# Performance work log

Hardware: AMD Instinct MI355X
Metric: run time of the kernel (lower is better)

## Reference

```python
import jax, jax.numpy as jnp
import numpy as np

D_MODEL = 1024
NHEAD = 16
D_K = D_MODEL // NHEAD


def setup_inputs() -> dict:
    key = jax.random.key(0)
    ks = jax.random.split(key, 11)
    B, S = 4, 2048
    s = 1.0 / np.sqrt(D_MODEL)
    return {
        "query": jax.random.normal(ks[0], (B, S, D_MODEL), jnp.float32),
        "key": jax.random.normal(ks[1], (B, S, D_MODEL), jnp.float32),
        "value": jax.random.normal(ks[2], (B, S, D_MODEL), jnp.float32),
        "wq": jax.random.normal(ks[3], (D_MODEL, D_MODEL), jnp.float32) * s,
        "bq": jnp.zeros((D_MODEL,), jnp.float32),
        "wk": jax.random.normal(ks[4], (D_MODEL, D_MODEL), jnp.float32) * s,
        "bk": jnp.zeros((D_MODEL,), jnp.float32),
        "wv": jax.random.normal(ks[5], (D_MODEL, D_MODEL), jnp.float32) * s,
        "bv": jnp.zeros((D_MODEL,), jnp.float32),
        "wo": jax.random.normal(ks[6], (D_MODEL, D_MODEL), jnp.float32) * s,
        "bo": jnp.zeros((D_MODEL,), jnp.float32),
    }


def reference(query, key, value, wq, bq, wk, bk, wv, bv, wo, bo):
    B, Sq, _ = query.shape
    Sk = key.shape[1]
    scale = 1.0 / np.sqrt(D_K).astype(np.float32)
    # projections, split into heads: [B, H, S, d_k]
    Q = (query @ wq.T + bq).reshape(B, Sq, NHEAD, D_K).transpose(0, 2, 1, 3)
    K = (key @ wk.T + bk).reshape(B, Sk, NHEAD, D_K).transpose(0, 2, 1, 3)
    V = (value @ wv.T + bv).reshape(B, Sk, NHEAD, D_K).transpose(0, 2, 1, 3)
    scores = jnp.einsum('bhqd,bhkd->bhqk', Q, K) * scale
    attn = jax.nn.softmax(scores, axis=-1)  # dropout p=0 (eval)
    ctx = jnp.einsum('bhqk,bhkd->bhqd', attn, V)
    ctx = ctx.transpose(0, 2, 1, 3).reshape(B, Sq, D_MODEL)
    return ctx @ wo.T + bo
```

## Files before the change

### kernel.cpp

```cpp
#include <hip/hip_runtime.h>
#include <math.h>

#define D_MODEL 1024
#define NHEAD   16
#define DK      64
#define BATCH   4
#define SEQ     2048
#define MROWS   8192

typedef __attribute__((ext_vector_type(4)))  float f32x4;
typedef __attribute__((ext_vector_type(16))) float f32x16;
typedef __attribute__((ext_vector_type(8)))  short bf16x8;

#define QSCALE 0.18033688011112042f

__device__ __forceinline__ unsigned int cvt_pk_bf16(float lo, float hi) {
  unsigned int r;
  asm("v_cvt_pk_bf16_f32 %0, %1, %2" : "=v"(r) : "v"(lo), "v"(hi));
  return r;
}

__global__ __launch_bounds__(256) void cvt_all(
    const float* __restrict__ q, const float* __restrict__ k, const float* __restrict__ v,
    const float* __restrict__ wq, const float* __restrict__ wk,
    const float* __restrict__ wv, const float* __restrict__ wo,
    unsigned short* __restrict__ qb, unsigned short* __restrict__ kb,
    unsigned short* __restrict__ vb, unsigned short* __restrict__ wqb,
    unsigned short* __restrict__ wkb, unsigned short* __restrict__ wvb,
    unsigned short* __restrict__ wob) {
  const int bid = blockIdx.x;
  const float* src; unsigned short* dst; int off;
  if      (bid < 4096)  { src = q;  dst = qb;  off = bid; }
  else if (bid < 8192)  { src = k;  dst = kb;  off = bid - 4096; }
  else if (bid < 12288) { src = v;  dst = vb;  off = bid - 8192; }
  else if (bid < 12800) { src = wq; dst = wqb; off = bid - 12288; }
  else if (bid < 13312) { src = wk; dst = wkb; off = bid - 12800; }
  else if (bid < 13824) { src = wv; dst = wvb; off = bid - 13312; }
  else                  { src = wo; dst = wob; off = bid - 13824; }
  const size_t i = (size_t)off * 256 + threadIdx.x;
  const float4* p = (const float4*)src + i * 2;
  const float4 a = p[0], b = p[1];
  int4 o;
  o.x = (int)cvt_pk_bf16(a.x, a.y);
  o.y = (int)cvt_pk_bf16(a.z, a.w);
  o.z = (int)cvt_pk_bf16(b.x, b.y);
  o.w = (int)cvt_pk_bf16(b.z, b.w);
  *(int4*)(dst + i * 8) = o;
}

__global__ __launch_bounds__(256) void gemm_qkv(
    const unsigned short* __restrict__ Aq, const unsigned short* __restrict__ Ak,
    const unsigned short* __restrict__ Av,
    const unsigned short* __restrict__ Wq, const unsigned short* __restrict__ Wk,
    const unsigned short* __restrict__ Wv,
    const float* __restrict__ bq, const float* __restrict__ bk,
    const float* __restrict__ bv,
    unsigned short* __restrict__ Qo, unsigned short* __restrict__ Ko,
    unsigned short* __restrict__ Vo) {
  __shared__ unsigned short Asb[128 * 32];
  __shared__ unsigned short Bsb[128 * 32];
  const int t = threadIdx.x;
  const int lane = t & 63, w = t >> 6;
  const int wr = w >> 1, wc = w & 1;
  const int g = lane >> 4, cl = lane & 15;
  const int id = blockIdx.x;
  const int jj = id >> 3;
  const int my = (id & 7) * 8 + (jj & 7);
  const int xs = jj >> 3;
  const int sector = xs >> 3;
  const int n0 = (xs & 7) * 128;
  const int m0 = my * 128;
  const unsigned short* A = sector == 0 ? Aq : sector == 1 ? Ak : Av;
  const unsigned short* W = sector == 0 ? Wq : sector == 1 ? Wk : Wv;
  const float* bias = sector == 0 ? bq : sector == 1 ? bk : bv;

  f32x4 acc[4][4];
#pragma unroll
  for (int i = 0; i < 4; ++i)
#pragma unroll
    for (int j = 0; j < 4; ++j) acc[i][j] = (f32x4){0.f, 0.f, 0.f, 0.f};

  for (int k0 = 0; k0 < D_MODEL; k0 += 32) {
    __syncthreads();
#pragma unroll
    for (int p = 0; p < 2; ++p) {
      const int c = p * 256 + t;
      const unsigned short* ga = A + (size_t)(m0 + (c >> 2)) * D_MODEL + k0 + (c & 3) * 8;
      const unsigned short* gw = W + (size_t)(n0 + (c >> 2)) * D_MODEL + k0 + (c & 3) * 8;
      __builtin_amdgcn_global_load_lds(
          (const __attribute__((address_space(1))) unsigned int*)ga,
          (__attribute__((address_space(3))) unsigned int*)(Asb + (size_t)c * 8), 16, 0, 0);
      __builtin_amdgcn_global_load_lds(
          (const __attribute__((address_space(1))) unsigned int*)gw,
          (__attribute__((address_space(3))) unsigned int*)(Bsb + (size_t)c * 8), 16, 0, 0);
    }
    __syncthreads();

    bf16x8 af[4], bfr[4];
#pragma unroll
    for (int mi = 0; mi < 4; ++mi)
      af[mi] = *(const bf16x8*)&Asb[(wr * 64 + mi * 16 + cl) * 32 + g * 8];
#pragma unroll
    for (int ni = 0; ni < 4; ++ni)
      bfr[ni] = *(const bf16x8*)&Bsb[(wc * 64 + ni * 16 + cl) * 32 + g * 8];
#pragma unroll
    for (int mi = 0; mi < 4; ++mi)
#pragma unroll
      for (int ni = 0; ni < 4; ++ni)
        acc[mi][ni] = __builtin_amdgcn_mfma_f32_16x16x32_bf16(af[mi], bfr[ni], acc[mi][ni], 0, 0, 0);
  }

  if (sector < 2) {
    unsigned short* O = sector == 0 ? Qo : Ko;
    const float sc = sector == 0 ? QSCALE : 1.0f;
#pragma unroll
    for (int mi = 0; mi < 4; ++mi)
#pragma unroll
      for (int ni = 0; ni < 4; ++ni) {
        const int nn = n0 + wc * 64 + ni * 16 + cl;
        const int hh = nn >> 6, d = nn & 63;
        const float bvv = bias[nn];
#pragma unroll
        for (int j = 0; j < 4; ++j) {
          const int mm = m0 + wr * 64 + mi * 16 + 4 * g + j;
          const int b = mm >> 11, s = mm & (SEQ - 1);
          const float v = (acc[mi][ni][j] + bvv) * sc;
          O[(((size_t)(b * NHEAD + hh) * SEQ) + s) * DK + d] = (unsigned short)cvt_pk_bf16(v, v);
        }
      }
  } else {
#pragma unroll
    for (int mi = 0; mi < 4; ++mi)
#pragma unroll
      for (int ni = 0; ni < 4; ++ni) {
        const int nn = n0 + wc * 64 + ni * 16 + cl;
        const int hh = nn >> 6, d = nn & 63;
        const float bvv = bias[nn];
        const int mmb = m0 + wr * 64 + mi * 16 + 4 * g;
        const int b = mmb >> 11, s = mmb & (SEQ - 1);
        uint2 w2;
        w2.x = cvt_pk_bf16(acc[mi][ni][0] + bvv, acc[mi][ni][1] + bvv);
        w2.y = cvt_pk_bf16(acc[mi][ni][2] + bvv, acc[mi][ni][3] + bvv);
        *(uint2*)&Vo[(((size_t)(b * NHEAD + hh)) * DK + d) * SEQ + s] = w2;
      }
  }
}

__global__ __launch_bounds__(256) void gemm_out(const unsigned short* __restrict__ A,
                                                const unsigned short* __restrict__ W,
                                                const float* __restrict__ bias,
                                                float* __restrict__ C) {
  __shared__ unsigned short Asb[128 * 32];
  __shared__ unsigned short Bsb[128 * 32];
  const int t = threadIdx.x;
  const int lane = t & 63, w = t >> 6;
  const int wr = w >> 1, wc = w & 1;
  const int g = lane >> 4, cl = lane & 15;
  const int id = blockIdx.x;
  const int jj = id >> 3;
  const int my = (id & 7) * 8 + (jj & 7);
  const int m0 = my * 128, n0 = (jj >> 3) * 128;

  f32x4 acc[4][4];
#pragma unroll
  for (int i = 0; i < 4; ++i)
#pragma unroll
    for (int j = 0; j < 4; ++j) acc[i][j] = (f32x4){0.f, 0.f, 0.f, 0.f};

  for (int k0 = 0; k0 < D_MODEL; k0 += 32) {
    __syncthreads();
#pragma unroll
    for (int p = 0; p < 2; ++p) {
      const int c = p * 256 + t;
      const unsigned short* ga = A + (size_t)(m0 + (c >> 2)) * D_MODEL + k0 + (c & 3) * 8;
      const unsigned short* gw = W + (size_t)(n0 + (c >> 2)) * D_MODEL + k0 + (c & 3) * 8;
      __builtin_amdgcn_global_load_lds(
          (const __attribute__((address_space(1))) unsigned int*)ga,
          (__attribute__((address_space(3))) unsigned int*)(Asb + (size_t)c * 8), 16, 0, 0);
      __builtin_amdgcn_global_load_lds(
          (const __attribute__((address_space(1))) unsigned int*)gw,
          (__attribute__((address_space(3))) unsigned int*)(Bsb + (size_t)c * 8), 16, 0, 0);
    }
    __syncthreads();

    bf16x8 af[4], bfr[4];
#pragma unroll
    for (int mi = 0; mi < 4; ++mi)
      af[mi] = *(const bf16x8*)&Asb[(wr * 64 + mi * 16 + cl) * 32 + g * 8];
#pragma unroll
    for (int ni = 0; ni < 4; ++ni)
      bfr[ni] = *(const bf16x8*)&Bsb[(wc * 64 + ni * 16 + cl) * 32 + g * 8];
#pragma unroll
    for (int mi = 0; mi < 4; ++mi)
#pragma unroll
      for (int ni = 0; ni < 4; ++ni)
        acc[mi][ni] = __builtin_amdgcn_mfma_f32_16x16x32_bf16(af[mi], bfr[ni], acc[mi][ni], 0, 0, 0);
  }

#pragma unroll
  for (int mi = 0; mi < 4; ++mi)
#pragma unroll
    for (int ni = 0; ni < 4; ++ni) {
      const int nn = n0 + wc * 64 + ni * 16 + cl;
      const float bvv = bias[nn];
#pragma unroll
      for (int j = 0; j < 4; ++j) {
        const int mm = m0 + wr * 64 + mi * 16 + 4 * g + j;
        C[(size_t)mm * D_MODEL + nn] = acc[mi][ni][j] + bvv;
      }
    }
}

__global__ __launch_bounds__(256) void attn_mfma(const unsigned short* __restrict__ Qh,
                                                 const unsigned short* __restrict__ Kh,
                                                 const unsigned short* __restrict__ Vt,
                                                 unsigned short* __restrict__ Ctx) {
  __shared__ unsigned short Ks[2][64 * 64];
  __shared__ unsigned short Vs[2][64 * 64];

  const int t = threadIdx.x;
  const int lane = t & 63, w = t >> 6;
  const int q32 = lane & 31, h = lane >> 5;
  const int xm = q32 & 7;

  const int id = blockIdx.x;
  const int jj = id >> 3;
  const int bh = (id & 7) * 8 + (jj & 7);
  const int qt = jj >> 3;
  const int q0 = qt * 128 + w * 32;

  const unsigned short* Qp = Qh + ((size_t)bh * SEQ + q0) * DK;
  const unsigned short* Kp = Kh + (size_t)bh * SEQ * DK;
  const unsigned short* Vp = Vt + (size_t)bh * DK * SEQ;

  const int cc0 = t, cc1 = 256 + t;
  const int sr0 = cc0 >> 3, sr1 = cc1 >> 3;
  const unsigned short* kp0 = Kp + sr0 * DK  + (((cc0 & 7) ^ (sr0 & 7)) << 3);
  const unsigned short* kp1 = Kp + sr1 * DK  + (((cc1 & 7) ^ (sr1 & 7)) << 3);
  const unsigned short* vp0 = Vp + sr0 * SEQ + (((cc0 & 7) ^ (sr0 & 7)) << 3);
  const unsigned short* vp1 = Vp + sr1 * SEQ + (((cc1 & 7) ^ (sr1 & 7)) << 3);

  auto stage = [&](int buf) {
    __builtin_amdgcn_global_load_lds(
        (const __attribute__((address_space(1))) unsigned int*)kp0,
        (__attribute__((address_space(3))) unsigned int*)(&Ks[buf][cc0 * 8]), 16, 0, 0);
    __builtin_amdgcn_global_load_lds(
        (const __attribute__((address_space(1))) unsigned int*)kp1,
        (__attribute__((address_space(3))) unsigned int*)(&Ks[buf][cc1 * 8]), 16, 0, 0);
    __builtin_amdgcn_global_load_lds(
        (const __attribute__((address_space(1))) unsigned int*)vp0,
        (__attribute__((address_space(3))) unsigned int*)(&Vs[buf][cc0 * 8]), 16, 0, 0);
    __builtin_amdgcn_global_load_lds(
        (const __attribute__((address_space(1))) unsigned int*)vp1,
        (__attribute__((address_space(3))) unsigned int*)(&Vs[buf][cc1 * 8]), 16, 0, 0);
    kp0 += 64 * DK; kp1 += 64 * DK;
    vp0 += 64;      vp1 += 64;
  };

  bf16x8 qf[4];
#pragma unroll
  for (int dc = 0; dc < 4; ++dc)
    qf[dc] = *(const bf16x8*)&Qp[(size_t)q32 * DK + dc * 16 + h * 8];

  f32x16 oc[2];
#pragma unroll
  for (int d0 = 0; d0 < 2; ++d0)
#pragma unroll
    for (int r = 0; r < 16; ++r) oc[d0][r] = 0.f;
  float m = -1e30f, lsum = 0.f;

  auto compute = [&](int buf) {
    const char* Kb = (const char*)&Ks[buf][0];
    const char* Vb = (const char*)&Vs[buf][0];

    f32x16 st0, st1;
#pragma unroll
    for (int r = 0; r < 16; ++r) { st0[r] = 0.f; st1[r] = 0.f; }
    __builtin_amdgcn_s_setprio(1);
#pragma unroll
    for (int dc = 0; dc < 4; ++dc) {
      const bf16x8 kf0 = *(const bf16x8*)(Kb + (q32)*128      + (((dc * 2 + h) ^ xm) << 4));
      st0 = __builtin_amdgcn_mfma_f32_32x32x16_bf16(kf0, qf[dc], st0, 0, 0, 0);
      const bf16x8 kf1 = *(const bf16x8*)(Kb + (32 + q32)*128 + (((dc * 2 + h) ^ xm) << 4));
      st1 = __builtin_amdgcn_mfma_f32_32x32x16_bf16(kf1, qf[dc], st1, 0, 0, 0);
    }
    __builtin_amdgcn_s_setprio(0);

    float tmx[8];
#pragma unroll
    for (int r = 0; r < 8; ++r)
      tmx[r] = fmaxf(fmaxf(st0[r], st0[r + 8]), fmaxf(st1[r], st1[r + 8]));
    const float a0 = fmaxf(fmaxf(tmx[0], tmx[1]), tmx[2]);
    const float a1 = fmaxf(fmaxf(tmx[3], tmx[4]), tmx[5]);
    const float a2 = fmaxf(tmx[6], tmx[7]);
    float pmax = fmaxf(fmaxf(a0, a1), a2);
    pmax = fmaxf(pmax, __shfl_xor(pmax, 32));

    if (!__all(pmax - m <= 8.0f)) {
      const float mnew = fmaxf(m, pmax);
      const float fsc = __builtin_amdgcn_exp2f(m - mnew);
      m = mnew;
      lsum *= fsc;
#pragma unroll
      for (int d0 = 0; d0 < 2; ++d0)
#pragma unroll
        for (int r = 0; r < 16; ++r) oc[d0][r] *= fsc;
    }

    float rs0 = 0.f, rs1 = 0.f, rs2 = 0.f, rs3 = 0.f;
#pragma unroll
    for (int r = 0; r < 16; ++r) {
      const float p0 = __builtin_amdgcn_exp2f(st0[r] - m);
      st0[r] = p0;
      const float p1 = __builtin_amdgcn_exp2f(st1[r] - m);
      st1[r] = p1;
      if ((r & 3) == 0) rs0 += p0 + p1;
      else if ((r & 3) == 1) rs1 += p0 + p1;
      else if ((r & 3) == 2) rs2 += p0 + p1;
      else rs3 += p0 + p1;
    }
    lsum += (rs0 + rs1) + (rs2 + rs3);

    int4 pv[4];
    {
      auto s0 = __builtin_amdgcn_permlane32_swap(
          cvt_pk_bf16(st0[0], st0[1]), cvt_pk_bf16(st0[4], st0[5]), false, false);
      auto s1 = __builtin_amdgcn_permlane32_swap(
          cvt_pk_bf16(st0[2], st0[3]), cvt_pk_bf16(st0[6], st0[7]), false, false);
      pv[0] = (int4){(int)s0[0], (int)s1[0], (int)s0[1], (int)s1[1]};
      auto s2 = __builtin_amdgcn_permlane32_swap(
          cvt_pk_bf16(st0[8], st0[9]), cvt_pk_bf16(st0[12], st0[13]), false, false);
      auto s3 = __builtin_amdgcn_permlane32_swap(
          cvt_pk_bf16(st0[10], st0[11]), cvt_pk_bf16(st0[14], st0[15]), false, false);
      pv[1] = (int4){(int)s2[0], (int)s3[0], (int)s2[1], (int)s3[1]};
      auto s4 = __builtin_amdgcn_permlane32_swap(
          cvt_pk_bf16(st1[0], st1[1]), cvt_pk_bf16(st1[4], st1[5]), false, false);
      auto s5 = __builtin_amdgcn_permlane32_swap(
          cvt_pk_bf16(st1[2], st1[3]), cvt_pk_bf16(st1[6], st1[7]), false, false);
      pv[2] = (int4){(int)s4[0], (int)s5[0], (int)s4[1], (int)s5[1]};
      auto s6 = __builtin_amdgcn_permlane32_swap(
          cvt_pk_bf16(st1[8], st1[9]), cvt_pk_bf16(st1[12], st1[13]), false, false);
      auto s7 = __builtin_amdgcn_permlane32_swap(
          cvt_pk_bf16(st1[10], st1[11]), cvt_pk_bf16(st1[14], st1[15]), false, false);
      pv[3] = (int4){(int)s6[0], (int)s7[0], (int)s6[1], (int)s7[1]};
    }

    __builtin_amdgcn_s_setprio(1);
#pragma unroll
    for (int ks = 0; ks < 4; ++ks) {
      union { int4 i; bf16x8 v; } pu;
      pu.i = pv[ks];
#pragma unroll
      for (int d0 = 0; d0 < 2; ++d0) {
        const bf16x8 vf = *(const bf16x8*)(Vb + (d0 * 32 + q32) * 128 + (((ks * 2 + h) ^ xm) << 4));
        oc[d0] = __builtin_amdgcn_mfma_f32_32x32x16_bf16(vf, pu.v, oc[d0], 0, 0, 0);
      }
    }
    __builtin_amdgcn_s_setprio(0);
  };

  stage(0);
  __syncthreads();
#pragma unroll 1
  for (int kt = 0; kt < 30; kt += 2) {
    stage(1);
    compute(0);
    __syncthreads();
    stage(0);
    compute(1);
    __syncthreads();
  }
  stage(1);
  compute(0);
  __syncthreads();
  compute(1);

  lsum += __shfl_xor(lsum, 32);
  const float inv = 1.f / lsum;
  unsigned short* Cp = Ctx + ((size_t)(bh >> 4) * SEQ + q0 + q32) * D_MODEL + (bh & 15) * DK;
#pragma unroll
  for (int d0 = 0; d0 < 2; ++d0)
#pragma unroll
    for (int rq = 0; rq < 4; ++rq) {
      const int dbase = d0 * 32 + 8 * rq + 4 * h;
      uint2 w2;
      w2.x = cvt_pk_bf16(oc[d0][4 * rq + 0] * inv, oc[d0][4 * rq + 1] * inv);
      w2.y = cvt_pk_bf16(oc[d0][4 * rq + 2] * inv, oc[d0][4 * rq + 3] * inv);
      *(uint2*)(Cp + dbase) = w2;
    }
}

extern "C" void kernel_launch(void* const* d_in, const int* in_sizes, int n_in,
                              void* d_out, int out_size, void* d_ws, size_t ws_size,
                              hipStream_t stream) {
  const float* query = (const float*)d_in[0];
  const float* key   = (const float*)d_in[1];
  const float* value = (const float*)d_in[2];
  const float* wq = (const float*)d_in[3];
  const float* bq = (const float*)d_in[4];
  const float* wk = (const float*)d_in[5];
  const float* bk = (const float*)d_in[6];
  const float* wv = (const float*)d_in[7];
  const float* bv = (const float*)d_in[8];
  const float* wo = (const float*)d_in[9];
  const float* bo = (const float*)d_in[10];

  unsigned short* ws = (unsigned short*)d_ws;
  const size_t TA = (size_t)MROWS * D_MODEL;
  const size_t TW = (size_t)D_MODEL * D_MODEL;
  unsigned short* qb  = ws;
  unsigned short* kb  = qb + TA;
  unsigned short* vb  = kb + TA;
  unsigned short* wqb = vb + TA;
  unsigned short* wkb = wqb + TW;
  unsigned short* wvb = wkb + TW;
  unsigned short* wob = wvb + TW;
  unsigned short* Qh  = wob + TW;
  unsigned short* Kh  = Qh + TA;
  unsigned short* Vt  = Kh + TA;
  unsigned short* Cb  = Vt + TA;

  cvt_all<<<dim3(14336), 256, 0, stream>>>(query, key, value, wq, wk, wv, wo,
                                           qb, kb, vb, wqb, wkb, wvb, wob);
  gemm_qkv<<<dim3(1536), 256, 0, stream>>>(qb, kb, vb, wqb, wkb, wvb,
                                           bq, bk, bv, Qh, Kh, Vt);
  attn_mfma<<<dim3(1024), 256, 0, stream>>>(Qh, Kh, Vt, Cb);
  gemm_out<<<dim3(512), 256, 0, stream>>>(Cb, wob, bo, (float*)d_out);
}
```

Before: 353.5 us.

## Software-pipeline attention: overlap next tile QK with current softmax/PV, triple-buffer LDS

Splits the per-tile attention step into a QK^T score phase and a softmax-plus-PV phase. The score MFMAs for the next key tile are issued before the softmax and PV of the current tile, so matrix and vector work can overlap. LDS staging grows from double to triple buffering, and the main loop is unrolled into a six-step rotation to keep the same total of 32 key tiles. Holding two sets of score accumulators raises VGPR use, and the larger LDS footprint can reduce occupancy.

```diff
diff --git a/kernel.cpp b/kernel.cpp
--- a/kernel.cpp
+++ b/kernel.cpp
@@ -215,8 +215,8 @@
                                                  const unsigned short* __restrict__ Kh,
                                                  const unsigned short* __restrict__ Vt,
                                                  unsigned short* __restrict__ Ctx) {
-  __shared__ unsigned short Ks[2][64 * 64];
-  __shared__ unsigned short Vs[2][64 * 64];
+  __shared__ unsigned short Ks[3][64 * 64];
+  __shared__ unsigned short Vs[3][64 * 64];
 
   const int t = threadIdx.x;
   const int lane = t & 63, w = t >> 6;
@@ -269,23 +269,25 @@
     for (int r = 0; r < 16; ++r) oc[d0][r] = 0.f;
   float m = -1e30f, lsum = 0.f;
 
-  auto compute = [&](int buf) {
+  auto qk = [&](int buf, f32x16& s0out, f32x16& s1out) {
     const char* Kb = (const char*)&Ks[buf][0];
-    const char* Vb = (const char*)&Vs[buf][0];
-
-    f32x16 st0, st1;
-#pragma unroll
-    for (int r = 0; r < 16; ++r) { st0[r] = 0.f; st1[r] = 0.f; }
+    f32x16 a, b;
+#pragma unroll
+    for (int r = 0; r < 16; ++r) { a[r] = 0.f; b[r] = 0.f; }
     __builtin_amdgcn_s_setprio(1);
 #pragma unroll
     for (int dc = 0; dc < 4; ++dc) {
       const bf16x8 kf0 = *(const bf16x8*)(Kb + (q32)*128      + (((dc * 2 + h) ^ xm) << 4));
-      st0 = __builtin_amdgcn_mfma_f32_32x32x16_bf16(kf0, qf[dc], st0, 0, 0, 0);
+      a = __builtin_amdgcn_mfma_f32_32x32x16_bf16(kf0, qf[dc], a, 0, 0, 0);
       const bf16x8 kf1 = *(const bf16x8*)(Kb + (32 + q32)*128 + (((dc * 2 + h) ^ xm) << 4));
-      st1 = __builtin_amdgcn_mfma_f32_32x32x16_bf16(kf1, qf[dc], st1, 0, 0, 0);
+      b = __builtin_amdgcn_mfma_f32_32x32x16_bf16(kf1, qf[dc], b, 0, 0, 0);
     }
     __builtin_amdgcn_s_setprio(0);
-
+    s0out = a; s1out = b;
+  };
+
+  auto fin = [&](int vbuf, f32x16& st0, f32x16& st1) {
+    const char* Vb = (const char*)&Vs[vbuf][0];
     float tmx[8];
 #pragma unroll
     for (int r = 0; r < 8; ++r)
@@ -359,21 +361,26 @@
     __builtin_amdgcn_s_setprio(0);
   };
 
+  f32x16 stA0, stA1, stB0, stB1;
+
   stage(0);
+  stage(1);
   __syncthreads();
+  qk(0, stA0, stA1);
+
 #pragma unroll 1
-  for (int kt = 0; kt < 30; kt += 2) {
-    stage(1);
-    compute(0);
-    __syncthreads();
-    stage(0);
-    compute(1);
-    __syncthreads();
+  for (int it = 0; it < 5; ++it) {
+    stage(2); qk(1, stB0, stB1); fin(0, stA0, stA1); __syncthreads();
+    stage(0); qk(2, stA0, stA1); fin(1, stB0, stB1); __syncthreads();
+    stage(1); qk(0, stB0, stB1); fin(2, stA0, stA1); __syncthreads();
+    stage(2); qk(1, stA0, stA1); fin(0, stB0, stB1); __syncthreads();
+    stage(0); qk(2, stB0, stB1); fin(1, stA0, stA1); __syncthreads();
+    stage(1); qk(0, stA0, stA1); fin(2, stB0, stB1); __syncthreads();
   }
-  stage(1);
-  compute(0);
+  qk(1, stB0, stB1);
+  fin(0, stA0, stA1);
   __syncthreads();
-  compute(1);
+  fin(1, stB0, stB1);
 
   lsum += __shfl_xor(lsum, 32);
   const float inv = 1.f / lsum;
```

Measured after the change: 352.9 us. Within noise of the previous version (-0.2%).
